# Optimization experiments

Hardware: AMD Instinct MI355X
Metric: run time of the kernel (lower is better)

## Reference

```python
import jax, jax.numpy as jnp
import numpy as np

CODEBOOK_SIZE = 1024
LATENT_DIM = 64
BETA = 0.25      # commitment_beta
DECAY = 0.99     # ema_decay
EPS = 1e-5       # ema_eps
DIVERSITY_W = 1.0


def _hadamard(n):
    # Sylvester construction (n must be a power of 2)
    H = np.array([[1.0]], dtype=np.float32)
    while H.shape[0] < n:
        H = np.block([[H, H], [H, -H]])
    return H.astype(np.float32)


def setup_inputs() -> dict:
    key = jax.random.key(0)
    k1, k2, k3 = jax.random.split(key, 3)
    B, C, H, W = 32, LATENT_DIM, 32, 32
    x = jax.random.normal(k1, (B, C, H, W), dtype=jnp.float32)
    embedding_weight = jax.random.normal(k2, (CODEBOOK_SIZE, LATENT_DIM), dtype=jnp.float32)
    rotation_matrix = jnp.asarray(_hadamard(LATENT_DIM))
    ema_w = jax.random.normal(k3, (CODEBOOK_SIZE, LATENT_DIM), dtype=jnp.float32)
    ema_cluster_size = jnp.ones((CODEBOOK_SIZE,), dtype=jnp.float32)
    return {"x": x, "embedding_weight": embedding_weight,
            "rotation_matrix": rotation_matrix, "ema_w": ema_w,
            "ema_cluster_size": ema_cluster_size}


def reference(x, embedding_weight, rotation_matrix, ema_w, ema_cluster_size):
    B, C, H, W = x.shape
    K, D = embedding_weight.shape
    N = B * H * W
    sg = jax.lax.stop_gradient

    # flatten channel-last, rotate
    xf = jnp.transpose(x, (0, 2, 3, 1)).reshape(N, D)      # [N, D]
    xr = xf @ rotation_matrix                               # [N, D]

    # pairwise squared distances to codebook + argmin
    dist = (jnp.sum(xr * xr, axis=-1, keepdims=True)
            + jnp.sum(embedding_weight * embedding_weight, axis=-1)[None, :]
            - 2.0 * (xr @ embedding_weight.T))              # [N, K]
    idx = jnp.argmin(dist, axis=-1)                         # [N]

    # one-hot scatter equivalents (counts / dw) done with index scatter-add
    counts = jnp.zeros((K,), x.dtype).at[idx].add(1.0)      # encodings.sum(0)
    quant = embedding_weight[idx]                           # [N, D]
    # NOTE: original code views (B*H*W, C) row-major directly as (B, C, H, W)
    quant_out = quant.reshape(B, C, H, W)

    # EMA codebook update (training=True path)
    cs = ema_cluster_size * DECAY + (1.0 - DECAY) * counts
    n = jnp.sum(cs)
    cs = (cs + EPS) / (n + K * EPS) * n
    dw = jnp.zeros((K, D), x.dtype).at[idx].add(xr)         # encodings.T @ xr
    new_ema_w = ema_w * DECAY + (1.0 - DECAY) * dw
    new_embedding = new_ema_w / cs[:, None]

    commitment_loss = BETA * jnp.mean((sg(quant_out) - x) ** 2)
    codebook_loss = jnp.mean((quant_out - sg(x)) ** 2)

    # diversity: mean over ALL (i, j) pairs of ||e_i - xr_j||^2 (original
    # broadcasts (N,1,D) vs (N,D) -> (N,N,D)); identical closed form:
    e = new_embedding[idx]                                  # [N, D]
    diversity_loss = DIVERSITY_W * (jnp.mean(jnp.sum(e * e, axis=-1))
                                    + jnp.mean(jnp.sum(xr * xr, axis=-1))
                                    - 2.0 * jnp.dot(jnp.mean(e, axis=0), jnp.mean(xr, axis=0)))

    avg_probs = counts / N
    perplexity = jnp.exp(-jnp.sum(avg_probs * jnp.log(avg_probs + 1e-10)))

    quant_st = x + sg(quant_out - x)                        # straight-through
    return (quant_st, codebook_loss, commitment_loss, diversity_loss,
            perplexity, idx, cs, new_ema_w, new_embedding)
```

## Files before the change

kernel.cpp:

```cpp
#include <hip/hip_runtime.h>
#include <math.h>

#define NTOK 32768
#define KCB  1024
#define DIM  64
#define THETA 0.02f

typedef __attribute__((ext_vector_type(8))) short short8;
typedef __attribute__((ext_vector_type(4))) float f32x4;
#define MFMA __builtin_amdgcn_mfma_f32_16x16x32_bf16
#define ALOAD(p) __hip_atomic_load((p), __ATOMIC_RELAXED, __HIP_MEMORY_SCOPE_AGENT)

#define WS_XR      0
#define WS_ENORM   2097152
#define WS_EH      2098176
#define WS_EL      2130944
#define WS_COUNTS  2163712
#define WS_CS      2164736
#define WS_XRSUM   2165760
#define WS_ESUM    2166272
#define WS_SCALREP 2166784
#define WS_FLAGCNT 2166912
#define WS_IDX     2166928
#define WS_SORT    2199696
#define WS_OFF     2232464

#define O_Q    0
#define O_CB   2097152
#define O_CM   2097153
#define O_DV   2097154
#define O_PP   2097155
#define O_IDX  2097156
#define O_CS   2129924
#define O_EW   2130948
#define O_EMB  2196484

__device__ __forceinline__ void hilo(float v, unsigned &h, unsigned &l)
{
    unsigned b  = __float_as_uint(v);
    unsigned hb = (b + 0x7FFFu + ((b >> 16) & 1u)) & 0xFFFF0000u;
    float lof   = v - __uint_as_float(hb);
    unsigned lb = __float_as_uint(lof);
    l = (lb + 0x7FFFu + ((lb >> 16) & 1u)) >> 16;
    h = hb >> 16;
}

__global__ __launch_bounds__(256) void k_rotate_enorm(const float* __restrict__ x,
    const float* __restrict__ E, float* __restrict__ xr, float* __restrict__ enorm,
    unsigned short* __restrict__ eh, unsigned short* __restrict__ el,
    float* __restrict__ counts, int* __restrict__ flagc,
    float* __restrict__ e_sum, float* __restrict__ xr_sum,
    float* __restrict__ scalrep)
{
    int tid = threadIdx.x;
    if (blockIdx.x >= 512) {
        int b = (int)blockIdx.x - 512;
        counts[(b << 8) + tid] = 0.f;
        if (b == 0) {
            if (tid < 16) flagc[tid] = 0;
            if (tid < 128) scalrep[tid] = 0.f;
        } else if (b == 1) {
            e_sum[tid] = 0.f; e_sum[256 + tid] = 0.f;
        } else if (b == 2) {
            xr_sum[tid] = 0.f; xr_sum[256 + tid] = 0.f;
        }
        int k = (b << 8) + tid;
        const float* ep = E + ((size_t)k << 6);
        unsigned* ehw = (unsigned*)eh + (k << 5);
        unsigned* elw = (unsigned*)el + (k << 5);
        float s = 0.f;
        #pragma unroll
        for (int q = 0; q < 32; ++q) {
            float v0 = ep[2*q], v1 = ep[2*q+1];
            s = fmaf(v0, v0, s); s = fmaf(v1, v1, s);
            unsigned h0, l0, h1, l1;
            hilo(v0, h0, l0);
            hilo(v1, h1, l1);
            ehw[q] = h0 | (h1 << 16);
            elw[q] = l0 | (l1 << 16);
        }
        enorm[k] = s;
        return;
    }
    __shared__ float xt[64 * 65];
    int p  = blockIdx.x >> 4;
    int s0 = ((int)blockIdx.x & 15) << 6;

    {
        const float4* x4 = (const float4*)x;
        #pragma unroll
        for (int pass = 0; pass < 4; ++pass) {
            int q = (pass << 8) + tid;
            int c = q >> 4, col = (q & 15) << 2;
            float4 v = x4[(p << 14) + (c << 8) + (s0 >> 2) + (col >> 2)];
            float* dst = xt + c * 65 + col;
            dst[0] = v.x; dst[1] = v.y; dst[2] = v.z; dst[3] = v.w;
        }
    }
    __syncthreads();

    int lane = tid & 63, w = tid >> 6;
    #pragma unroll
    for (int i = 0; i < 4; ++i) {
        int sl = (w << 4) + (i << 2);
        const float* src = xt + lane * 65 + sl;
        float4 v = make_float4(src[0], src[1], src[2], src[3]);
        #pragma unroll
        for (int s = 1; s <= 32; s <<= 1) {
            float sgn = (lane & s) ? -1.f : 1.f;
            float ox = __shfl_xor(v.x, s);
            float oy = __shfl_xor(v.y, s);
            float oz = __shfl_xor(v.z, s);
            float ow = __shfl_xor(v.w, s);
            v.x = fmaf(sgn, v.x, ox);
            v.y = fmaf(sgn, v.y, oy);
            v.z = fmaf(sgn, v.z, oz);
            v.w = fmaf(sgn, v.w, ow);
        }
        int t0 = ((int)blockIdx.x << 6) + sl;
        float* dst = xr + ((size_t)t0 << 6) + lane;
        dst[0]   = v.x;
        dst[64]  = v.y;
        dst[128] = v.z;
        dst[192] = v.w;
    }
}

__global__ __launch_bounds__(256, 4) void k_argmin_fix(const float* __restrict__ xr,
    const unsigned short* __restrict__ eh, const unsigned short* __restrict__ el,
    const float* __restrict__ enorm, const float* __restrict__ E,
    const float* __restrict__ ecs, int* __restrict__ idxw,
    float* __restrict__ out_idx, float* __restrict__ counts,
    float* __restrict__ out_cs, float* __restrict__ csw,
    int* __restrict__ off, int* __restrict__ sorted, int* __restrict__ done_ctr)
{
    __shared__ uint4 ehs[1024];
    __shared__ uint4 els[1024];
    __shared__ float ens[128];
    __shared__ float m_b1[32], m_b2[32];
    __shared__ int   m_id[32];
    __shared__ int   finidx[32];
    __shared__ int   finflag[32];
    __shared__ unsigned fmask;
    int tid = threadIdx.x;
    int lane = tid & 63, w = tid >> 6;
    int ts = w >> 1, kh = w & 1;
    int tx = lane & 15, gq = lane >> 4;
    int n0 = (int)blockIdx.x << 5;
    int tokbase = n0 + (ts << 4);

    short8 ah0, al0, ah1, al1;
    {
        const float* xp = xr + ((size_t)(tokbase + tx) << 6) + (gq << 3);
        float4 xa = *(const float4*)(xp);
        float4 xb = *(const float4*)(xp + 4);
        float4 xc = *(const float4*)(xp + 32);
        float4 xd = *(const float4*)(xp + 36);
        float a0v[8] = {xa.x,xa.y,xa.z,xa.w,xb.x,xb.y,xb.z,xb.w};
        float a1v[8] = {xc.x,xc.y,xc.z,xc.w,xd.x,xd.y,xd.z,xd.w};
        #pragma unroll
        for (int j = 0; j < 8; ++j) {
            unsigned h, l;
            hilo(a0v[j], h, l);
            ah0[j] = (short)h; al0[j] = (short)l;
            hilo(a1v[j], h, l);
            ah1[j] = (short)h; al1[j] = (short)l;
        }
    }

    float b1[4], b2[4]; int idx[4];
    #pragma unroll
    for (int r = 0; r < 4; ++r) { b1[r] = 3.4e38f; b2[r] = 3.4e38f; idx[r] = 0; }

    int swz0 = gq ^ (tx & 7);
    int swz1 = (4 + gq) ^ (tx & 7);
    const f32x4 z4 = {0.f, 0.f, 0.f, 0.f};

    for (int ch = 0; ch < 8; ++ch) {
        int c0 = ch << 7;
        __syncthreads();
        {
            const uint4* ghs = (const uint4*)eh + ((size_t)c0 << 3);
            const uint4* gls = (const uint4*)el + ((size_t)c0 << 3);
            #pragma unroll
            for (int i = 0; i < 4; ++i) {
                int u = (i << 8) + tid;
                int rr = u >> 3, bb = u & 7;
                int bs = bb ^ (rr & 7);
                ehs[(rr << 3) + bs] = ghs[u];
                els[(rr << 3) + bs] = gls[u];
            }
            if (tid < 128) ens[tid] = enorm[c0 + tid];
        }
        __syncthreads();

        #pragma unroll
        for (int s = 0; s < 4; ++s) {
            int rbase = (kh << 6) + (s << 4) + tx;
            short8 bh0 = ((const short8*)ehs)[(rbase << 3) + swz0];
            short8 bh1 = ((const short8*)ehs)[(rbase << 3) + swz1];
            short8 bl0 = ((const short8*)els)[(rbase << 3) + swz0];
            short8 bl1 = ((const short8*)els)[(rbase << 3) + swz1];

            f32x4 a0 = MFMA(ah0, bh0, z4, 0, 0, 0);
            a0 = MFMA(ah0, bl0, a0, 0, 0, 0);
            a0 = MFMA(al0, bh0, a0, 0, 0, 0);
            f32x4 a1 = MFMA(ah1, bh1, z4, 0, 0, 0);
            a1 = MFMA(ah1, bl1, a1, 0, 0, 0);
            a1 = MFMA(al1, bh1, a1, 0, 0, 0);

            float en = ens[rbase];
            int kk = c0 + rbase;
            #pragma unroll
            for (int r = 0; r < 4; ++r) {
                float sv = fmaf(-2.f, a0[r], fmaf(-2.f, a1[r], en));
                float mx = fmaxf(sv, b1[r]);
                b2[r] = fminf(b2[r], mx);
                bool t = sv < b1[r];
                idx[r] = t ? kk : idx[r];
                b1[r] = fminf(b1[r], sv);
            }
        }
    }

    float v1f[4], v2f[4]; int idf[4];
    #pragma unroll
    for (int r = 0; r < 4; ++r) {
        float v1 = b1[r], v2 = b2[r]; int id = idx[r];
        #pragma unroll
        for (int m = 1; m <= 8; m <<= 1) {
            float o1 = __shfl_xor(v1, m);
            float o2 = __shfl_xor(v2, m);
            int   oi = __shfl_xor(id, m);
            float nb2 = fminf(fminf(v2, o2), fmaxf(v1, o1));
            bool t = (o1 < v1) || (o1 == v1 && oi < id);
            v1 = t ? o1 : v1;
            id = t ? oi : id;
            v2 = nb2;
        }
        v1f[r] = v1; v2f[r] = v2; idf[r] = id;
    }

    int tl = (ts << 4) + (gq << 2);
    if (kh == 1 && tx == 0) {
        #pragma unroll
        for (int r = 0; r < 4; ++r) {
            m_b1[tl + r] = v1f[r];
            m_b2[tl + r] = v2f[r];
            m_id[tl + r] = idf[r];
        }
    }
    __syncthreads();
    if (kh == 0 && tx == 0) {
        #pragma unroll
        for (int r = 0; r < 4; ++r) {
            float o1 = m_b1[tl + r], o2 = m_b2[tl + r];
            int   oi = m_id[tl + r];
            float v1 = v1f[r]; int id = idf[r];
            float b2m = fminf(fminf(v2f[r], o2), fmaxf(v1, o1));
            bool t = (o1 < v1) || (o1 == v1 && oi < id);
            float v1m = t ? o1 : v1;
            int   idm = t ? oi : id;
            finidx[tl + r]  = idm;
            finflag[tl + r] = (b2m - v1m < THETA) ? 1 : 0;
        }
    }
    __syncthreads();

    {
        int fl = (tid < 32) ? finflag[tid] : 0;
        unsigned long long bal = __ballot(fl != 0);
        if (tid == 0) fmask = (unsigned)bal;
    }
    __syncthreads();
    {
        unsigned msk = fmask;
        int widx = 0;
        while (msk) {
            int src = __ffs(msk) - 1; msk &= msk - 1;
            if ((widx++ & 3) != w) continue;
            int tok = n0 + src;
            const float4* xp = (const float4*)(xr + ((size_t)tok << 6));
            float best = 3.4e38f; int bidx = 0;
            for (int c = 0; c < 16; ++c) {
                int k = (c << 6) + lane;
                const float4* epp = (const float4*)(E + ((size_t)k << 6));
                float d = 0.f;
                #pragma unroll
                for (int q = 0; q < 16; ++q) {
                    float4 e = epp[q];
                    float4 xa = xp[q];
                    d = fmaf(xa.x, e.x, d);
                    d = fmaf(xa.y, e.y, d);
                    d = fmaf(xa.z, e.z, d);
                    d = fmaf(xa.w, e.w, d);
                }
                float sv = fmaf(-2.f, d, enorm[k]);
                if (sv < best) { best = sv; bidx = k; }
            }
            #pragma unroll
            for (int m = 1; m <= 32; m <<= 1) {
                float ov = __shfl_xor(best, m);
                int   oi = __shfl_xor(bidx, m);
                if (ov < best || (ov == best && oi < bidx)) { best = ov; bidx = oi; }
            }
            if (lane == 0) finidx[src] = bidx;
        }
    }
    __syncthreads();

    if (tid < 32) {
        int tok = n0 + tid;
        int idm = finidx[tid];
        atomicExch(&idxw[tok], idm);
        out_idx[tok] = (float)idm;
        atomicAdd(&counts[idm], 1.f);
    }

    __shared__ int ticket;
    __syncthreads();
    if (tid == 0) ticket = atomicAdd(done_ctr, 1);
    __syncthreads();
    if (ticket != 1023) return;

    int* soff = (int*)ehs;
    int* scur = soff + 1024;
    __shared__ int   wcnt2[4], woff2[4];
    __shared__ float wsum2[4];
    __shared__ float nss;

    int ci4[4]; int s = 0;
    float cs4[4]; float csum = 0.f;
    #pragma unroll
    for (int j = 0; j < 4; ++j) {
        int kk = (tid << 2) + j;
        float c = ALOAD(&counts[kk]);
        ci4[j] = (int)c;
        s += ci4[j];
        float cs = ecs[kk] * 0.99f + 0.01f * c;
        cs4[j] = cs;
        csum += cs;
    }
    int sc = s;
    #pragma unroll
    for (int o = 1; o < 64; o <<= 1) {
        int u = __shfl_up(sc, o);
        if (lane >= o) sc += u;
    }
    float v = csum;
    #pragma unroll
    for (int m = 32; m >= 1; m >>= 1) v += __shfl_xor(v, m);
    if (lane == 63) wcnt2[w] = sc;
    if (lane == 0)  wsum2[w] = v;
    __syncthreads();
    if (tid == 0) {
        int run = 0;
        #pragma unroll
        for (int i = 0; i < 4; ++i) { woff2[i] = run; run += wcnt2[i]; }
        nss = wsum2[0] + wsum2[1] + wsum2[2] + wsum2[3];
    }
    __syncthreads();
    float nn = nss;
    int run = woff2[w] + (sc - s);
    #pragma unroll
    for (int j = 0; j < 4; ++j) {
        int kk = (tid << 2) + j;
        off[kk] = run;
        soff[kk] = run;
        scur[kk] = run;
        run += ci4[j];
        float csf = (cs4[j] + 1e-5f) / (nn + 1024.f * 1e-5f) * nn;
        out_cs[kk] = csf;
        csw[kk] = csf;
    }
    __syncthreads();
    for (int t = tid; t < NTOK; t += 256) {
        int k = ALOAD(&idxw[t]);
        int pos = atomicAdd(&scur[k], 1);
        sorted[pos] = t;
    }
}

__global__ __launch_bounds__(256) void k_quant_dwemb(const float* __restrict__ x,
    const float* __restrict__ xr, const float* __restrict__ E,
    const int* __restrict__ idxw, const int* __restrict__ sorted,
    const int* __restrict__ off, const float* __restrict__ counts,
    const float* __restrict__ csw, const float* __restrict__ emaw,
    float* __restrict__ outq, float* __restrict__ out_ew,
    float* __restrict__ out_emb, float* __restrict__ e_sum,
    float* __restrict__ xr_sum, float* __restrict__ scalrep,
    float* __restrict__ out, int* __restrict__ done_ctr)
{
    __shared__ int   lidx[32];
    __shared__ float wr[4], wn[4];
    __shared__ float part[3][64];
    __shared__ int   seg[2048];
    int tid = threadIdx.x;
    int lane = tid & 63, w = tid >> 6;
    int k = blockIdx.x;

    int n0 = k << 5;
    if (tid < 32) lidx[tid] = idxw[n0 + tid];
    __syncthreads();
    int f40 = k << 9;
    float sq = 0.f, xn = 0.f;
    #pragma unroll
    for (int it = 0; it < 2; ++it) {
        int q = (it << 8) + tid;
        int kk = lidx[q >> 4];
        int d4 = q & 15;
        float4 xv = ((const float4*)x)[f40 + q];
        float4 ev = ((const float4*)E)[(kk << 4) + d4];
        float dx = ev.x - xv.x, dy = ev.y - xv.y, dz = ev.z - xv.z, dw_ = ev.w - xv.w;
        ((float4*)outq)[f40 + q] = make_float4(xv.x + dx, xv.y + dy, xv.z + dz, xv.w + dw_);
        sq += dx*dx + dy*dy + dz*dz + dw_*dw_;
        xn += xv.x*xv.x + xv.y*xv.y + xv.z*xv.z + xv.w*xv.w;
    }
    #pragma unroll
    for (int m = 32; m >= 1; m >>= 1) { sq += __shfl_xor(sq, m); xn += __shfl_xor(xn, m); }
    if (lane == 0) { wr[w] = sq; wn[w] = xn; }
    __syncthreads();
    if (tid == 0) {
        int rep = (k & 7) << 4;
        atomicAdd(&scalrep[rep + 0], wr[0] + wr[1] + wr[2] + wr[3]);
        atomicAdd(&scalrep[rep + 1], wn[0] + wn[1] + wn[2] + wn[3]);
    }

    int d = lane;
    int a = off[k];
    int cnt = (int)counts[k];
    int end = a + cnt;
    float sum = 0.f;
    for (int base = a; base < end; base += 2048) {
        int clen = min(2048, end - base);
        __syncthreads();
        for (int t = tid; t < clen; t += 256) seg[t] = sorted[base + t];
        __syncthreads();
        #pragma unroll 2
        for (int j = w; j < clen; j += 4) {
            int tok = seg[j];
            sum += xr[((size_t)tok << 6) + d];
        }
    }
    __syncthreads();
    if (w) part[w - 1][d] = sum;
    __syncthreads();
    if (w == 0) {
        float dw = sum + part[0][d] + part[1][d] + part[2][d];
        int i = (k << 6) + d;
        float nw = emaw[i] * 0.99f + 0.01f * dw;
        out_ew[i] = nw;
        float emb = nw / csw[k];
        out_emb[i] = emb;
        if (cnt > 0) {
            int rep = (k & 7) << 6;
            atomicAdd(&xr_sum[rep + d], dw);
            float c = (float)cnt;
            atomicAdd(&e_sum[rep + d], c * emb);
            float t2 = c * emb * emb;
            #pragma unroll
            for (int m = 32; m >= 1; m >>= 1) t2 += __shfl_xor(t2, m);
            if (d == 0) atomicAdd(&scalrep[((k & 7) << 4) + 2], t2);
        }
    }

    __shared__ int ticket;
    __syncthreads();
    if (tid == 0) ticket = atomicAdd(done_ctr, 1);
    __syncthreads();
    if (ticket != 1023) return;

    __shared__ float wt[4], wd[4];
    float tt = 0.f;
    #pragma unroll
    for (int j = 0; j < 4; ++j) {
        float aa = ALOAD(&counts[(tid << 2) + j]) * (1.f / 32768.f);
        tt += aa * logf(aa + 1e-10f);
    }
    float dc = 0.f;
    if (tid < 64) {
        float xs8 = 0.f, es8 = 0.f;
        #pragma unroll
        for (int r2 = 0; r2 < 8; ++r2) {
            xs8 += ALOAD(&xr_sum[(r2 << 6) + tid]);
            es8 += ALOAD(&e_sum[(r2 << 6) + tid]);
        }
        dc = es8 * xs8;
    }
    #pragma unroll
    for (int m = 32; m >= 1; m >>= 1) { tt += __shfl_xor(tt, m); dc += __shfl_xor(dc, m); }
    if (lane == 0) { wt[w] = tt; wd[w] = dc; }
    __syncthreads();
    if (tid == 0) {
        float S = wt[0] + wt[1] + wt[2] + wt[3];
        float Dt = wd[0] + wd[1] + wd[2] + wd[3];
        float sqs = 0.f, xns = 0.f, s2s = 0.f;
        #pragma unroll
        for (int r2 = 0; r2 < 8; ++r2) {
            sqs += ALOAD(&scalrep[(r2 << 4) + 0]);
            xns += ALOAD(&scalrep[(r2 << 4) + 1]);
            s2s += ALOAD(&scalrep[(r2 << 4) + 2]);
        }
        float cb = sqs * (1.f / 2097152.f);
        out[O_CB] = cb;
        out[O_CM] = 0.25f * cb;
        float inv = 1.f / 32768.f;
        out[O_DV] = s2s * inv + 64.f * xns * inv - 2.f * (Dt * inv * inv);
        out[O_PP] = expf(-S);
    }
}

extern "C" void kernel_launch(void* const* d_in, const int* in_sizes, int n_in,
                              void* d_out, int out_size, void* d_ws, size_t ws_size,
                              hipStream_t stream)
{
    const float* x    = (const float*)d_in[0];
    const float* E    = (const float*)d_in[1];
    const float* emaw = (const float*)d_in[3];
    const float* ecs  = (const float*)d_in[4];
    float* out = (float*)d_out;
    float* ws  = (float*)d_ws;
    int* flagc = (int*)(ws + WS_FLAGCNT);

    hipLaunchKernelGGL(k_rotate_enorm, dim3(516), dim3(256), 0, stream,
                       x, E, ws + WS_XR, ws + WS_ENORM,
                       (unsigned short*)(ws + WS_EH), (unsigned short*)(ws + WS_EL),
                       ws + WS_COUNTS, flagc,
                       ws + WS_ESUM, ws + WS_XRSUM, ws + WS_SCALREP);
    hipLaunchKernelGGL(k_argmin_fix, dim3(1024), dim3(256), 0, stream,
                       ws + WS_XR, (const unsigned short*)(ws + WS_EH),
                       (const unsigned short*)(ws + WS_EL), ws + WS_ENORM,
                       E, ecs, (int*)(ws + WS_IDX), out + O_IDX, ws + WS_COUNTS,
                       out + O_CS, ws + WS_CS, (int*)(ws + WS_OFF),
                       (int*)(ws + WS_SORT), flagc + 1);
    hipLaunchKernelGGL(k_quant_dwemb, dim3(1024), dim3(256), 0, stream,
                       x, ws + WS_XR, E, (const int*)(ws + WS_IDX),
                       (const int*)(ws + WS_SORT), (const int*)(ws + WS_OFF),
                       ws + WS_COUNTS, ws + WS_CS, emaw,
                       out + O_Q, out + O_EW, out + O_EMB,
                       ws + WS_ESUM, ws + WS_XRSUM, ws + WS_SCALREP,
                       out, flagc + 2);
}
```

Measured before the change: 115.9 us.

## Use three-way bf16 split MFMA and drop fp32 near-tie recheck path

Splits both operands into high/mid/low bf16 parts and accumulates six MFMA products per tile instead of three, so the distance scores are close to fp32. This removes the second-best tracking, the near-tie flagging and the scalar fp32 rescan over the full codebook for ambiguous tokens. The cost is double the MFMA work, an extra 1024x64 bf16 slice staged in LDS, and a lower occupancy hint (3 blocks instead of 4). Exact-tie behaviour now depends on the split precision alone, which risks argmin mismatches against the fp32 reference.

```diff
diff --git a/kernel.cpp b/kernel.cpp
--- a/kernel.cpp
+++ b/kernel.cpp
@@ -4,7 +4,6 @@
 #define NTOK 32768
 #define KCB  1024
 #define DIM  64
-#define THETA 0.02f
 
 typedef __attribute__((ext_vector_type(8))) short short8;
 typedef __attribute__((ext_vector_type(4))) float f32x4;
@@ -14,16 +13,17 @@
 #define WS_XR      0
 #define WS_ENORM   2097152
 #define WS_EH      2098176
-#define WS_EL      2130944
-#define WS_COUNTS  2163712
-#define WS_CS      2164736
-#define WS_XRSUM   2165760
-#define WS_ESUM    2166272
-#define WS_SCALREP 2166784
-#define WS_FLAGCNT 2166912
-#define WS_IDX     2166928
-#define WS_SORT    2199696
-#define WS_OFF     2232464
+#define WS_EM      2130944
+#define WS_EL      2163712
+#define WS_COUNTS  2196480
+#define WS_CS      2197504
+#define WS_XRSUM   2198528
+#define WS_ESUM    2199040
+#define WS_SCALREP 2199552
+#define WS_FLAGCNT 2199680
+#define WS_IDX     2199696
+#define WS_SORT    2232464
+#define WS_OFF     2265232
 
 #define O_Q    0
 #define O_CB   2097152
@@ -35,19 +35,24 @@
 #define O_EW   2130948
 #define O_EMB  2196484
 
-__device__ __forceinline__ void hilo(float v, unsigned &h, unsigned &l)
+__device__ __forceinline__ void hilo3(float v, unsigned &h, unsigned &m, unsigned &l)
 {
     unsigned b  = __float_as_uint(v);
     unsigned hb = (b + 0x7FFFu + ((b >> 16) & 1u)) & 0xFFFF0000u;
-    float lof   = v - __uint_as_float(hb);
-    unsigned lb = __float_as_uint(lof);
-    l = (lb + 0x7FFFu + ((lb >> 16) & 1u)) >> 16;
+    float r1    = v - __uint_as_float(hb);
+    unsigned b1 = __float_as_uint(r1);
+    unsigned mb = (b1 + 0x7FFFu + ((b1 >> 16) & 1u)) & 0xFFFF0000u;
+    float r2    = r1 - __uint_as_float(mb);
+    unsigned b2 = __float_as_uint(r2);
+    l = (b2 + 0x7FFFu + ((b2 >> 16) & 1u)) >> 16;
     h = hb >> 16;
+    m = mb >> 16;
 }
 
 __global__ __launch_bounds__(256) void k_rotate_enorm(const float* __restrict__ x,
     const float* __restrict__ E, float* __restrict__ xr, float* __restrict__ enorm,
-    unsigned short* __restrict__ eh, unsigned short* __restrict__ el,
+    unsigned short* __restrict__ eh, unsigned short* __restrict__ em,
+    unsigned short* __restrict__ el,
     float* __restrict__ counts, int* __restrict__ flagc,
     float* __restrict__ e_sum, float* __restrict__ xr_sum,
     float* __restrict__ scalrep)
@@ -67,16 +72,18 @@
         int k = (b << 8) + tid;
         const float* ep = E + ((size_t)k << 6);
         unsigned* ehw = (unsigned*)eh + (k << 5);
+        unsigned* emw = (unsigned*)em + (k << 5);
         unsigned* elw = (unsigned*)el + (k << 5);
         float s = 0.f;
         #pragma unroll
         for (int q = 0; q < 32; ++q) {
             float v0 = ep[2*q], v1 = ep[2*q+1];
             s = fmaf(v0, v0, s); s = fmaf(v1, v1, s);
-            unsigned h0, l0, h1, l1;
-            hilo(v0, h0, l0);
-            hilo(v1, h1, l1);
+            unsigned h0, m0, l0, h1, m1, l1;
+            hilo3(v0, h0, m0, l0);
+            hilo3(v1, h1, m1, l1);
             ehw[q] = h0 | (h1 << 16);
+            emw[q] = m0 | (m1 << 16);
             elw[q] = l0 | (l1 << 16);
         }
         enorm[k] = s;
@@ -126,22 +133,20 @@
     }
 }
 
-__global__ __launch_bounds__(256, 4) void k_argmin_fix(const float* __restrict__ xr,
-    const unsigned short* __restrict__ eh, const unsigned short* __restrict__ el,
-    const float* __restrict__ enorm, const float* __restrict__ E,
+__global__ __launch_bounds__(256, 3) void k_argmin(const float* __restrict__ xr,
+    const unsigned short* __restrict__ eh, const unsigned short* __restrict__ em,
+    const unsigned short* __restrict__ el, const float* __restrict__ enorm,
     const float* __restrict__ ecs, int* __restrict__ idxw,
     float* __restrict__ out_idx, float* __restrict__ counts,
     float* __restrict__ out_cs, float* __restrict__ csw,
     int* __restrict__ off, int* __restrict__ sorted, int* __restrict__ done_ctr)
 {
     __shared__ uint4 ehs[1024];
+    __shared__ uint4 ems[1024];
     __shared__ uint4 els[1024];
     __shared__ float ens[128];
-    __shared__ float m_b1[32], m_b2[32];
+    __shared__ float m_b1[32];
     __shared__ int   m_id[32];
-    __shared__ int   finidx[32];
-    __shared__ int   finflag[32];
-    __shared__ unsigned fmask;
     int tid = threadIdx.x;
     int lane = tid & 63, w = tid >> 6;
     int ts = w >> 1, kh = w & 1;
@@ -149,7 +154,7 @@
     int n0 = (int)blockIdx.x << 5;
     int tokbase = n0 + (ts << 4);
 
-    short8 ah0, al0, ah1, al1;
+    short8 ah0, am0, al0, ah1, am1, al1;
     {
         const float* xp = xr + ((size_t)(tokbase + tx) << 6) + (gq << 3);
         float4 xa = *(const float4*)(xp);
@@ -160,17 +165,17 @@
         float a1v[8] = {xc.x,xc.y,xc.z,xc.w,xd.x,xd.y,xd.z,xd.w};
         #pragma unroll
         for (int j = 0; j < 8; ++j) {
-            unsigned h, l;
-            hilo(a0v[j], h, l);
-            ah0[j] = (short)h; al0[j] = (short)l;
-            hilo(a1v[j], h, l);
-            ah1[j] = (short)h; al1[j] = (short)l;
-        }
-    }
-
-    float b1[4], b2[4]; int idx[4];
-    #pragma unroll
-    for (int r = 0; r < 4; ++r) { b1[r] = 3.4e38f; b2[r] = 3.4e38f; idx[r] = 0; }
+            unsigned h, m, l;
+            hilo3(a0v[j], h, m, l);
+            ah0[j] = (short)h; am0[j] = (short)m; al0[j] = (short)l;
+            hilo3(a1v[j], h, m, l);
+            ah1[j] = (short)h; am1[j] = (short)m; al1[j] = (short)l;
+        }
+    }
+
+    float b1[4]; int idx[4];
+    #pragma unroll
+    for (int r = 0; r < 4; ++r) { b1[r] = 3.4e38f; idx[r] = 0; }
 
     int swz0 = gq ^ (tx & 7);
     int swz1 = (4 + gq) ^ (tx & 7);
@@ -181,6 +186,7 @@
         __syncthreads();
         {
             const uint4* ghs = (const uint4*)eh + ((size_t)c0 << 3);
+            const uint4* gms = (const uint4*)em + ((size_t)c0 << 3);
             const uint4* gls = (const uint4*)el + ((size_t)c0 << 3);
             #pragma unroll
             for (int i = 0; i < 4; ++i) {
@@ -188,6 +194,7 @@
                 int rr = u >> 3, bb = u & 7;
                 int bs = bb ^ (rr & 7);
                 ehs[(rr << 3) + bs] = ghs[u];
+                ems[(rr << 3) + bs] = gms[u];
                 els[(rr << 3) + bs] = gls[u];
             }
             if (tid < 128) ens[tid] = enorm[c0 + tid];
@@ -199,23 +206,29 @@
             int rbase = (kh << 6) + (s << 4) + tx;
             short8 bh0 = ((const short8*)ehs)[(rbase << 3) + swz0];
             short8 bh1 = ((const short8*)ehs)[(rbase << 3) + swz1];
+            short8 bm0 = ((const short8*)ems)[(rbase << 3) + swz0];
+            short8 bm1 = ((const short8*)ems)[(rbase << 3) + swz1];
             short8 bl0 = ((const short8*)els)[(rbase << 3) + swz0];
             short8 bl1 = ((const short8*)els)[(rbase << 3) + swz1];
 
-            f32x4 a0 = MFMA(ah0, bh0, z4, 0, 0, 0);
+            f32x4 a0 = MFMA(al0, bh0, z4, 0, 0, 0);
             a0 = MFMA(ah0, bl0, a0, 0, 0, 0);
-            a0 = MFMA(al0, bh0, a0, 0, 0, 0);
-            f32x4 a1 = MFMA(ah1, bh1, z4, 0, 0, 0);
+            a0 = MFMA(am0, bm0, a0, 0, 0, 0);
+            a0 = MFMA(am0, bh0, a0, 0, 0, 0);
+            a0 = MFMA(ah0, bm0, a0, 0, 0, 0);
+            a0 = MFMA(ah0, bh0, a0, 0, 0, 0);
+            f32x4 a1 = MFMA(al1, bh1, z4, 0, 0, 0);
             a1 = MFMA(ah1, bl1, a1, 0, 0, 0);
-            a1 = MFMA(al1, bh1, a1, 0, 0, 0);
+            a1 = MFMA(am1, bm1, a1, 0, 0, 0);
+            a1 = MFMA(am1, bh1, a1, 0, 0, 0);
+            a1 = MFMA(ah1, bm1, a1, 0, 0, 0);
+            a1 = MFMA(ah1, bh1, a1, 0, 0, 0);
 
             float en = ens[rbase];
             int kk = c0 + rbase;
             #pragma unroll
             for (int r = 0; r < 4; ++r) {
                 float sv = fmaf(-2.f, a0[r], fmaf(-2.f, a1[r], en));
-                float mx = fmaxf(sv, b1[r]);
-                b2[r] = fminf(b2[r], mx);
                 bool t = sv < b1[r];
                 idx[r] = t ? kk : idx[r];
                 b1[r] = fminf(b1[r], sv);
@@ -223,22 +236,17 @@
         }
     }
 
-    float v1f[4], v2f[4]; int idf[4];
+    float v1f[4]; int idf[4];
     #pragma unroll
     for (int r = 0; r < 4; ++r) {
-        float v1 = b1[r], v2 = b2[r]; int id = idx[r];
+        float v1 = b1[r]; int id = idx[r];
         #pragma unroll
         for (int m = 1; m <= 8; m <<= 1) {
             float o1 = __shfl_xor(v1, m);
-            float o2 = __shfl_xor(v2, m);
             int   oi = __shfl_xor(id, m);
-            float nb2 = fminf(fminf(v2, o2), fmaxf(v1, o1));
-            bool t = (o1 < v1) || (o1 == v1 && oi < id);
-            v1 = t ? o1 : v1;
-            id = t ? oi : id;
-            v2 = nb2;
-        }
-        v1f[r] = v1; v2f[r] = v2; idf[r] = id;
+            if (o1 < v1 || (o1 == v1 && oi < id)) { v1 = o1; id = oi; }
+        }
+        v1f[r] = v1; idf[r] = id;
     }
 
     int tl = (ts << 4) + (gq << 2);
@@ -246,7 +254,6 @@
         #pragma unroll
         for (int r = 0; r < 4; ++r) {
             m_b1[tl + r] = v1f[r];
-            m_b2[tl + r] = v2f[r];
             m_id[tl + r] = idf[r];
         }
     }
@@ -254,67 +261,16 @@
     if (kh == 0 && tx == 0) {
         #pragma unroll
         for (int r = 0; r < 4; ++r) {
-            float o1 = m_b1[tl + r], o2 = m_b2[tl + r];
+            float o1 = m_b1[tl + r];
             int   oi = m_id[tl + r];
             float v1 = v1f[r]; int id = idf[r];
-            float b2m = fminf(fminf(v2f[r], o2), fmaxf(v1, o1));
             bool t = (o1 < v1) || (o1 == v1 && oi < id);
-            float v1m = t ? o1 : v1;
-            int   idm = t ? oi : id;
-            finidx[tl + r]  = idm;
-            finflag[tl + r] = (b2m - v1m < THETA) ? 1 : 0;
-        }
-    }
-    __syncthreads();
-
-    {
-        int fl = (tid < 32) ? finflag[tid] : 0;
-        unsigned long long bal = __ballot(fl != 0);
-        if (tid == 0) fmask = (unsigned)bal;
-    }
-    __syncthreads();
-    {
-        unsigned msk = fmask;
-        int widx = 0;
-        while (msk) {
-            int src = __ffs(msk) - 1; msk &= msk - 1;
-            if ((widx++ & 3) != w) continue;
-            int tok = n0 + src;
-            const float4* xp = (const float4*)(xr + ((size_t)tok << 6));
-            float best = 3.4e38f; int bidx = 0;
-            for (int c = 0; c < 16; ++c) {
-                int k = (c << 6) + lane;
-                const float4* epp = (const float4*)(E + ((size_t)k << 6));
-                float d = 0.f;
-                #pragma unroll
-                for (int q = 0; q < 16; ++q) {
-                    float4 e = epp[q];
-                    float4 xa = xp[q];
-                    d = fmaf(xa.x, e.x, d);
-                    d = fmaf(xa.y, e.y, d);
-                    d = fmaf(xa.z, e.z, d);
-                    d = fmaf(xa.w, e.w, d);
-                }
-                float sv = fmaf(-2.f, d, enorm[k]);
-                if (sv < best) { best = sv; bidx = k; }
-            }
-            #pragma unroll
-            for (int m = 1; m <= 32; m <<= 1) {
-                float ov = __shfl_xor(best, m);
-                int   oi = __shfl_xor(bidx, m);
-                if (ov < best || (ov == best && oi < bidx)) { best = ov; bidx = oi; }
-            }
-            if (lane == 0) finidx[src] = bidx;
-        }
-    }
-    __syncthreads();
-
-    if (tid < 32) {
-        int tok = n0 + tid;
-        int idm = finidx[tid];
-        atomicExch(&idxw[tok], idm);
-        out_idx[tok] = (float)idm;
-        atomicAdd(&counts[idm], 1.f);
+            int idm = t ? oi : id;
+            int tok = tokbase + (gq << 2) + r;
+            atomicExch(&idxw[tok], idm);
+            out_idx[tok] = (float)idm;
+            atomicAdd(&counts[idm], 1.f);
+        }
     }
 
     __shared__ int ticket;
@@ -524,13 +480,15 @@
 
     hipLaunchKernelGGL(k_rotate_enorm, dim3(516), dim3(256), 0, stream,
                        x, E, ws + WS_XR, ws + WS_ENORM,
-                       (unsigned short*)(ws + WS_EH), (unsigned short*)(ws + WS_EL),
+                       (unsigned short*)(ws + WS_EH), (unsigned short*)(ws + WS_EM),
+                       (unsigned short*)(ws + WS_EL),
                        ws + WS_COUNTS, flagc,
                        ws + WS_ESUM, ws + WS_XRSUM, ws + WS_SCALREP);
-    hipLaunchKernelGGL(k_argmin_fix, dim3(1024), dim3(256), 0, stream,
+    hipLaunchKernelGGL(k_argmin, dim3(1024), dim3(256), 0, stream,
                        ws + WS_XR, (const unsigned short*)(ws + WS_EH),
+                       (const unsigned short*)(ws + WS_EM),
                        (const unsigned short*)(ws + WS_EL), ws + WS_ENORM,
-                       E, ecs, (int*)(ws + WS_IDX), out + O_IDX, ws + WS_COUNTS,
+                       ecs, (int*)(ws + WS_IDX), out + O_IDX, ws + WS_COUNTS,
                        out + O_CS, ws + WS_CS, (int*)(ws + WS_OFF),
                        (int*)(ws + WS_SORT), flagc + 1);
     hipLaunchKernelGGL(k_quant_dwemb, dim3(1024), dim3(256), 0, stream,
```

Result: slower. 129.6 us (+11.9%).
